# Optimization experiments

Measured on AMD Instinct MI355X. Metric: run time of the kernel, lower is better.

## Reference

```python
import jax, jax.numpy as jnp
import numpy as np
import math

S, B, H, NH, I, L, V, BK, MP = 512, 8, 768, 12, 2304, 4, 16384, 32, 512
DH = H // NH   # 64
DV = I // NH   # 192
EPS = 1e-7
SCALE = 1.0 / math.sqrt(3 * DH)


def make_log_bucket_position(relative_pos, bucket_size, max_position):
    sign = np.sign(relative_pos)
    mid = bucket_size // 2
    abs_pos = np.where((relative_pos < mid) & (relative_pos > -mid),
                       mid - 1,
                       np.clip(np.abs(relative_pos), None, max_position - 1))
    log_pos = np.ceil(np.log(abs_pos / mid) / math.log((max_position - 1) / mid) * (mid - 1)).astype(np.int64) + mid
    bucket_pos = np.where(abs_pos <= mid, relative_pos, log_pos * sign).astype(np.int64)
    return bucket_pos


def layer_norm(x, eps=EPS):
    m = jnp.mean(x, axis=-1, keepdims=True)
    v = jnp.var(x, axis=-1, keepdims=True)
    return (x - m) / jnp.sqrt(v + eps)


def setup_inputs() -> dict:
    key = jax.random.key(0)
    ks = jax.random.split(key, 10)
    std = math.sqrt(2.0 / (5.0 * H))
    inp = {}
    inp['input_ids'] = jax.random.randint(ks[0], (S, B), 0, V, dtype=jnp.int32)
    inp['attention_mask'] = jnp.zeros((B, 1, 1, S), dtype=bool)
    rel = np.arange(S)[:, None] - np.arange(S)[None, :]
    rel = make_log_bucket_position(rel, BK, MP)
    inp['position_indices'] = jnp.asarray(BK - 1 + rel, dtype=jnp.int32)  # [S,S] in [0, 2*BK-2]
    inp['word_emb'] = jax.random.normal(ks[1], (V, H), jnp.float32) * std
    inp['rel_emb'] = jax.random.normal(ks[2], (2 * BK - 1, H), jnp.float32) * std
    inp['rel_ln_w'] = jnp.ones((H,), jnp.float32)
    inp['rel_ln_b'] = jnp.zeros((H,), jnp.float32)
    inp['Wv'] = jax.random.normal(ks[3], (L, 2 * I, H), jnp.float32) * std
    inp['Wqk'] = jax.random.normal(ks[4], (L, 2 * H, H), jnp.float32) * std
    inp['bqk'] = jnp.zeros((L, 2 * H), jnp.float32)
    inp['Wo'] = jax.random.normal(ks[5], (L, H, I), jnp.float32) * std
    inp['l_skip'] = jnp.zeros((L, I), jnp.float32)
    return inp


def attention_glu_layer(x, mask, rel, pos_idx, Wv, Wqk, bqk, Wo, l_skip):
    # x: [S,B,H]; rel: [2*BK-1, H]; mask: [B,1,1,S] bool (True = masked)
    h = layer_norm(x)
    vg = jnp.einsum('sbh,ih->sbi', h, Wv)                  # [S,B,2I]
    value, gate = jnp.split(vg, 2, axis=-1)
    gate = jax.nn.gelu(gate, approximate=False)
    value_skip = jax.nn.gelu(value, approximate=False)
    qk = jnp.einsum('sbh,ih->sbi', h, Wqk) + bqk            # [S,B,2H]
    q, k = jnp.split(qk, 2, axis=-1)
    # relative position projections
    pos = rel @ Wqk.T + bqk                                 # [2*BK-1, 2H]
    pos = pos[pos_idx]                                      # [S,S,2H]
    q_pos, k_pos = jnp.split(pos, 2, axis=-1)
    q_pos = q_pos.reshape(S, S, NH, DH)
    k_pos = k_pos.reshape(S, S, NH, DH)
    q4 = q.reshape(S, B, NH, DH)
    k4 = k.reshape(S, B, NH, DH)
    v4 = value.reshape(S, B, NH, DV)
    scores = jnp.einsum('qbhd,kbhd->bhqk', q4, k4) * SCALE
    scores = scores + jnp.einsum('qbhd,qkhd->bhqk', q4, k_pos) * SCALE
    scores = scores + jnp.einsum('kbhd,qkhd->bhqk', k4, q_pos) * SCALE
    scores = jnp.where(mask, -jnp.inf, scores)
    probs = jax.nn.softmax(scores, axis=-1)
    probs = jnp.where(mask, 0.0, probs)
    ctx = jnp.einsum('bhqk,kbhv->qbhv', probs, v4).reshape(S, B, I)
    ctx = ctx + jax.nn.sigmoid(l_skip) * value_skip
    ctx = ctx * gate
    ctx = layer_norm(ctx)
    out = jnp.einsum('sbi,hi->sbh', ctx, Wo)
    return x + out


def reference(input_ids, attention_mask, position_indices, word_emb, rel_emb,
              rel_ln_w, rel_ln_b, Wv, Wqk, bqk, Wo, l_skip):
    x = layer_norm(word_emb[input_ids])                      # [S,B,H]
    rel = layer_norm(rel_emb) * rel_ln_w + rel_ln_b          # [2*BK-1, H]
    for l in range(L):
        x = attention_glu_layer(x, attention_mask, rel, position_indices,
                                Wv[l], Wqk[l], bqk[l], Wo[l], l_skip[l])
    return x
```

## Files before the change

### kernel.cpp

```cpp
#include <hip/hip_runtime.h>
#include <hip/hip_bf16.h>
#include <math.h>

#define S 512
#define B 8
#define H 768
#define NH 12
#define DH 64
#define DV 192
#define II 2304
#define NL 4
#define SCALE 0.07216878364870322f
#define EPS 1e-7f

#define NW0 (2*II*H)
#define NW1 (2*H*H)
#define NW2 (H*II)

typedef __attribute__((ext_vector_type(8))) short short8;
typedef __attribute__((ext_vector_type(4))) float f32x4;

__device__ __forceinline__ float b2f(ushort u){
  union { float f; unsigned int u; } v; v.u = ((unsigned int)u) << 16; return v.f;
}
__device__ __forceinline__ ushort f2b(float f){
  union { float f; unsigned int u; } v; v.f = f;
  unsigned int u = v.u;
  return (ushort)((u + 0x7fffu + ((u >> 16) & 1u)) >> 16);
}
__device__ __forceinline__ float gelu_f(float x){
  return 0.5f * x * (1.0f + erff(x * 0.70710678118654752f));
}
__device__ __forceinline__ void async_copy16(const ushort* g, ushort* l){
  __builtin_amdgcn_global_load_lds(
      (const __attribute__((address_space(1))) void*)g,
      (__attribute__((address_space(3))) void*)l, 16, 0, 0);
}

__device__ __forceinline__ void block_sum2(float& s, float& s2, float* red, int t){
  #pragma unroll
  for(int off=32; off>=1; off>>=1){ s += __shfl_xor(s, off); s2 += __shfl_xor(s2, off); }
  int w = t >> 6;
  if((t & 63) == 0){ red[w] = s; red[4 + w] = s2; }
  __syncthreads();
  s  = red[0] + red[1] + red[2] + red[3];
  s2 = red[4] + red[5] + red[6] + red[7];
}

__global__ __launch_bounds__(256)
void f2b3_kernel(const float* __restrict__ in0, const float* __restrict__ in1,
                 const float* __restrict__ in2, ushort* __restrict__ out){
  int i = (blockIdx.x * 256 + threadIdx.x) * 4;
  const float* src; int off;
  if(i < NW0){ src = in0; off = i; }
  else if(i < NW0+NW1){ src = in1; off = i - NW0; }
  else { src = in2; off = i - NW0 - NW1; }
  float4 v = *(const float4*)(src + off);
  __attribute__((aligned(8))) ushort tmp[4] = { f2b(v.x), f2b(v.y), f2b(v.z), f2b(v.w) };
  *(uint2*)(out + i) = *(const uint2*)tmp;
}

__global__ __launch_bounds__(256)
void embed_ln_kernel(const int* __restrict__ ids, const float* __restrict__ wemb,
                     float* __restrict__ x)
{
  __shared__ float red[8];
  const int sb = blockIdx.x, t = threadIdx.x;
  const float* row = wemb + (size_t)ids[sb] * H;
  float v0 = row[t], v1 = row[t+256], v2 = row[t+512];
  float s = v0+v1+v2, s2 = v0*v0+v1*v1+v2*v2;
  block_sum2(s, s2, red, t);
  float mean = s * (1.0f/H);
  float rstd = rsqrtf(s2*(1.0f/H) - mean*mean + EPS);
  float* xo = x + (size_t)sb * H;
  xo[t]     = (v0-mean)*rstd;
  xo[t+256] = (v1-mean)*rstd;
  xo[t+512] = (v2-mean)*rstd;
}

__global__ __launch_bounds__(256)
void rel_ln_kernel(const float* __restrict__ rel_emb, const float* __restrict__ w,
                   const float* __restrict__ bia, ushort* __restrict__ outb)
{
  __shared__ float red[8];
  const int j = blockIdx.x, t = threadIdx.x;
  const float* row = rel_emb + (size_t)j * H;
  float v0=row[t], v1=row[t+256], v2=row[t+512];
  float s=v0+v1+v2, s2=v0*v0+v1*v1+v2*v2;
  block_sum2(s,s2,red,t);
  float mean = s*(1.0f/H);
  float rstd = rsqrtf(s2*(1.0f/H)-mean*mean+EPS);
  ushort* o = outb + (size_t)j*H;
  o[t]     = f2b((v0-mean)*rstd * w[t]     + bia[t]);
  o[t+256] = f2b((v1-mean)*rstd * w[t+256] + bia[t+256]);
  o[t+512] = f2b((v2-mean)*rstd * w[t+512] + bia[t+512]);
}

__global__ __launch_bounds__(256)
void ln_x_kernel(const float* __restrict__ x, ushort* __restrict__ h)
{
  __shared__ float red[8];
  const int sb = blockIdx.x, t = threadIdx.x;
  const float* row = x + (size_t)sb * H;
  float v0 = row[t], v1 = row[t+256], v2 = row[t+512];
  float s = v0+v1+v2, s2 = v0*v0+v1*v1+v2*v2;
  block_sum2(s, s2, red, t);
  float mean = s * (1.0f/H);
  float rstd = rsqrtf(s2*(1.0f/H) - mean*mean + EPS);
  ushort* o = h + (size_t)sb * H;
  o[t]     = f2b((v0-mean)*rstd);
  o[t+256] = f2b((v1-mean)*rstd);
  o[t+512] = f2b((v2-mean)*rstd);
}

__global__ __launch_bounds__(256)
void gemm_nt64(const ushort* __restrict__ A, const ushort* __restrict__ Bw,
               const float* __restrict__ bias, ushort* __restrict__ Cout,
               int M, int N, int K)
{
  __shared__ ushort As[64][40];
  __shared__ ushort Bs[64][40];
  const int n0 = blockIdx.x * 64, m0 = blockIdx.y * 64;
  const int t = threadIdx.x;
  const int lrow = t >> 2, lk = (t & 3) * 8;
  const int lane = t & 63, w = t >> 6, lr = lane & 15, lq = lane >> 4;
  const int wr = (w >> 1) * 32, wc = (w & 1) * 32;
  f32x4 z = {0.f,0.f,0.f,0.f};
  f32x4 acc[2][2] = {{z,z},{z,z}};
  const int arow = m0 + lrow;
  const ushort* aptr = A  + (size_t)arow * K + lk;
  const ushort* bptr = Bw + (size_t)(n0 + lrow) * K + lk;
  for(int k0 = 0; k0 < K; k0 += 32){
    short8 av = {0,0,0,0,0,0,0,0};
    if(arow < M) av = *(const short8*)(aptr + k0);
    short8 bv = *(const short8*)(bptr + k0);
    __syncthreads();
    *(short8*)&As[lrow][lk] = av;
    *(short8*)&Bs[lrow][lk] = bv;
    __syncthreads();
    short8 a0 = *(const short8*)&As[wr + lr][lq * 8];
    short8 a1 = *(const short8*)&As[wr + 16 + lr][lq * 8];
    short8 b0 = *(const short8*)&Bs[wc + lr][lq * 8];
    short8 b1 = *(const short8*)&Bs[wc + 16 + lr][lq * 8];
    acc[0][0] = __builtin_amdgcn_mfma_f32_16x16x32_bf16(a0, b0, acc[0][0], 0,0,0);
    acc[0][1] = __builtin_amdgcn_mfma_f32_16x16x32_bf16(a0, b1, acc[0][1], 0,0,0);
    acc[1][0] = __builtin_amdgcn_mfma_f32_16x16x32_bf16(a1, b0, acc[1][0], 0,0,0);
    acc[1][1] = __builtin_amdgcn_mfma_f32_16x16x32_bf16(a1, b1, acc[1][1], 0,0,0);
  }
  #pragma unroll
  for(int i=0;i<2;i++){
    #pragma unroll
    for(int j=0;j<2;j++){
      #pragma unroll
      for(int r=0;r<4;r++){
        int m = m0 + wr + i*16 + lq*4 + r;
        int n = n0 + wc + j*16 + lr;
        if(m >= M) continue;
        float v = acc[i][j][r];
        if(bias) v += bias[n];
        Cout[(size_t)m*N + n] = f2b(v);
      }
    }
  }
}

template<int OUT_MODE>
__global__ __launch_bounds__(256)
void gemm128(const ushort* __restrict__ A, const ushort* __restrict__ Bw,
             const float* __restrict__ bias, void* __restrict__ Cout,
             int M, int N, int K)
{
  __shared__ ushort As[128*32];
  __shared__ ushort Bs[128*32];
  const int t = threadIdx.x, w = t>>6, lane = t&63, lr = lane&15, lq = lane>>4;
  const int m0 = blockIdx.y*128, n0 = blockIdx.x*128;
  const int wr = (w>>1)*64, wc = (w&1)*64;
  const int srow = (w*2)*16 + (lane>>2);
  const int sk = (lane&3)*8;
  const ushort* aG = A  + (size_t)(m0+srow)*K + sk;
  const ushort* bG = Bw + (size_t)(n0+srow)*K + sk;
  ushort* aL0 = As + (w*2)*512;
  ushort* aL1 = As + (w*2+1)*512;
  ushort* bL0 = Bs + (w*2)*512;
  ushort* bL1 = Bs + (w*2+1)*512;
  f32x4 z = {0.f,0.f,0.f,0.f};
  f32x4 acc[4][4] = {{z,z,z,z},{z,z,z,z},{z,z,z,z},{z,z,z,z}};
  for(int k0 = 0; k0 < K; k0 += 32){
    __syncthreads();
    async_copy16(aG + k0,                 aL0);
    async_copy16(aG + k0 + (size_t)16*K,  aL1);
    async_copy16(bG + k0,                 bL0);
    async_copy16(bG + k0 + (size_t)16*K,  bL1);
    __syncthreads();
    short8 af[4], bf[4];
    #pragma unroll
    for(int i=0;i<4;i++) af[i] = *(const short8*)&As[(wr + i*16 + lr)*32 + lq*8];
    #pragma unroll
    for(int j=0;j<4;j++) bf[j] = *(const short8*)&Bs[(wc + j*16 + lr)*32 + lq*8];
    #pragma unroll
    for(int i=0;i<4;i++)
      #pragma unroll
      for(int j=0;j<4;j++)
        acc[i][j] = __builtin_amdgcn_mfma_f32_16x16x32_bf16(af[i], bf[j], acc[i][j], 0,0,0);
  }
  #pragma unroll
  for(int i=0;i<4;i++){
    #pragma unroll
    for(int j=0;j<4;j++){
      #pragma unroll
      for(int r=0;r<4;r++){
        int m = m0 + wr + i*16 + lq*4 + r;
        int n = n0 + wc + j*16 + lr;
        float v = acc[i][j][r];
        if(bias) v += bias[n];
        if(OUT_MODE == 0)      ((float*) Cout)[(size_t)m*N + n] = v;
        else if(OUT_MODE == 1) ((ushort*)Cout)[(size_t)m*N + n] = f2b(v);
        else                   ((float*) Cout)[(size_t)m*N + n] += v;
      }
    }
  }
}

__global__ __launch_bounds__(256)
void gemm_vgqk(const ushort* __restrict__ A, const ushort* __restrict__ Ww,
               const float* __restrict__ bqk, ushort* __restrict__ vg,
               ushort* __restrict__ qk)
{
  const int K = H;
  __shared__ ushort As[128*32];
  __shared__ ushort Bs[128*32];
  const int t = threadIdx.x, w = t>>6, lane = t&63, lr = lane&15, lq = lane>>4;
  const int m0 = blockIdx.y*128, n0 = blockIdx.x*128;
  const int wr = (w>>1)*64, wc = (w&1)*64;
  const int srow = (w*2)*16 + (lane>>2);
  const int sk = (lane&3)*8;
  const ushort* aG = A  + (size_t)(m0+srow)*K + sk;
  const ushort* bG = Ww + (size_t)(n0+srow)*K + sk;
  ushort* aL0 = As + (w*2)*512;
  ushort* aL1 = As + (w*2+1)*512;
  ushort* bL0 = Bs + (w*2)*512;
  ushort* bL1 = Bs + (w*2+1)*512;
  f32x4 z = {0.f,0.f,0.f,0.f};
  f32x4 acc[4][4] = {{z,z,z,z},{z,z,z,z},{z,z,z,z},{z,z,z,z}};
  for(int k0 = 0; k0 < K; k0 += 32){
    __syncthreads();
    async_copy16(aG + k0,                 aL0);
    async_copy16(aG + k0 + (size_t)16*K,  aL1);
    async_copy16(bG + k0,                 bL0);
    async_copy16(bG + k0 + (size_t)16*K,  bL1);
    __syncthreads();
    short8 af[4], bf[4];
    #pragma unroll
    for(int i=0;i<4;i++) af[i] = *(const short8*)&As[(wr + i*16 + lr)*32 + lq*8];
    #pragma unroll
    for(int j=0;j<4;j++) bf[j] = *(const short8*)&Bs[(wc + j*16 + lr)*32 + lq*8];
    #pragma unroll
    for(int i=0;i<4;i++)
      #pragma unroll
      for(int j=0;j<4;j++)
        acc[i][j] = __builtin_amdgcn_mfma_f32_16x16x32_bf16(af[i], bf[j], acc[i][j], 0,0,0);
  }
  const bool is_qk = (n0 >= 2*II);
  #pragma unroll
  for(int i=0;i<4;i++){
    #pragma unroll
    for(int j=0;j<4;j++){
      #pragma unroll
      for(int r=0;r<4;r++){
        int m = m0 + wr + i*16 + lq*4 + r;
        int n = n0 + wc + j*16 + lr;
        float v = acc[i][j][r];
        if(is_qk){
          int nq = n - 2*II;
          qk[(size_t)m*(2*H) + nq] = f2b(v + bqk[nq]);
        } else {
          vg[(size_t)m*(2*II) + n] = f2b(v);
        }
      }
    }
  }
}

__global__ __launch_bounds__(256)
void cpq_mfma2_kernel(const ushort* __restrict__ qk, const ushort* __restrict__ posb,
                      ushort* __restrict__ cpT, ushort* __restrict__ cqT)
{
  const int kc = blockIdx.x;
  const int bh = blockIdx.y;
  const int bb = bh / NH, h = bh - bb*NH;
  const int which = blockIdx.z;
  const int t = threadIdx.x, w = t>>6, lane = t&63, lr = lane&15, lq = lane>>4;
  const ushort* ab = posb + (size_t)(w*16 + lr)*1536 + (which ? 0 : 768) + h*64;
  short8 a0 = *(const short8*)(ab + lq*8);
  short8 a1 = *(const short8*)(ab + 32 + lq*8);
  f32x4 z = {0.f,0.f,0.f,0.f};
  f32x4 acc[8] = {z,z,z,z,z,z,z,z};
  #pragma unroll
  for(int nt=0; nt<8; nt++){
    const int k = kc*128 + nt*16 + lr;
    const ushort* bp = qk + ((size_t)k*B + bb)*1536 + (which ? 768 : 0) + h*64;
    short8 b0 = *(const short8*)(bp + lq*8);
    short8 b1 = *(const short8*)(bp + 32 + lq*8);
    acc[nt] = __builtin_amdgcn_mfma_f32_16x16x32_bf16(a0, b0, acc[nt], 0,0,0);
    acc[nt] = __builtin_amdgcn_mfma_f32_16x16x32_bf16(a1, b1, acc[nt], 0,0,0);
  }
  ushort* outp = which ? cqT : cpT;
  #pragma unroll
  for(int nt=0; nt<8; nt++){
    #pragma unroll
    for(int r=0;r<4;r++){
      int j = w*16 + lq*4 + r;
      int k = kc*128 + nt*16 + lr;
      outp[((size_t)bh*64 + j)*512 + k] = f2b(acc[nt][r]);
    }
  }
}

__global__ __launch_bounds__(256)
void vt_kernel(const ushort* __restrict__ vg, ushort* __restrict__ vt)
{
  const int st = blockIdx.x, hh = blockIdx.y, b = blockIdx.z;
  __shared__ ushort tile[32][200];
  const int t = threadIdx.x;
  {
    int sl = t >> 3, v0 = (t & 7) * 24;
    const ushort* src = vg + ((size_t)((st*32 + sl)*B + b))*(2*II) + hh*DV + v0;
    *(short8*)&tile[sl][v0]      = *(const short8*)(src);
    *(short8*)&tile[sl][v0 + 8]  = *(const short8*)(src + 8);
    *(short8*)&tile[sl][v0 + 16] = *(const short8*)(src + 16);
  }
  __syncthreads();
  if(t < DV){
    __attribute__((aligned(16))) ushort tmp[32];
    #pragma unroll
    for(int s2=0;s2<32;s2++) tmp[s2] = tile[s2][t];
    ushort* dst = vt + (((size_t)(b*NH + hh))*DV + t)*S + st*32;
    #pragma unroll
    for(int c=0;c<32;c+=8) *(short8*)(dst + c) = *(const short8*)&tmp[c];
  }
}

__global__ __launch_bounds__(256)
void attn_kernel(const ushort* __restrict__ qk, const ushort* __restrict__ vt,
                 const ushort* __restrict__ cpT, const ushort* __restrict__ cqT,
                 const int* __restrict__ pidx, ushort* __restrict__ ctx)
{
  const int bh = blockIdx.x, qt = blockIdx.y;
  const int b = bh / NH, hh = bh - b*NH;
  __shared__ ushort Qs[32][72];
  __shared__ ushort Ps[32][520];
  __shared__ float cps[32][65];
  __shared__ float redm[4][32];
  __shared__ float reds[4][32];
  __shared__ float rowinv[32];
  const int t = threadIdx.x, w = t>>6, lane = t&63, lr = lane&15, lq = lane>>4;

  for(int i=t; i<512; i+=256){
    int r = i >> 4, d0 = (i & 15) * 4;
    const ushort* src = qk + ((size_t)((qt*32 + r)*B + b))*1536 + hh*DH + d0;
    *(uint2*)&Qs[r][d0] = *(const uint2*)src;
  }
  for(int i=t; i<32*64; i+=256){
    int j = i >> 5, r = i & 31;
    cps[r][j] = b2f(cpT[((size_t)bh*64 + j)*512 + qt*32 + r]);
  }
  __syncthreads();

  short8 a00 = *(const short8*)&Qs[lr][lq*8];
  short8 a01 = *(const short8*)&Qs[lr][32 + lq*8];
  short8 a10 = *(const short8*)&Qs[16 + lr][lq*8];
  short8 a11 = *(const short8*)&Qs[16 + lr][32 + lq*8];

  float sc[8][8];
  const int kbase = w * 128;
  const ushort* cqbase = cqT + (size_t)bh*64*512;
  f32x4 z4 = {0.f,0.f,0.f,0.f};
  #pragma unroll
  for(int tile=0; tile<8; tile++){
    const int k0 = kbase + tile*16;
    const ushort* kp = qk + ((size_t)((k0 + lr)*B + b))*1536 + H + hh*DH + lq*8;
    short8 b0 = *(const short8*)kp;
    short8 b1 = *(const short8*)(kp + 32);
    f32x4 acc[2] = {z4, z4};
    acc[0] = __builtin_amdgcn_mfma_f32_16x16x32_bf16(a00, b0, acc[0], 0,0,0);
    acc[0] = __builtin_amdgcn_mfma_f32_16x16x32_bf16(a01, b1, acc[0], 0,0,0);
    acc[1] = __builtin_amdgcn_mfma_f32_16x16x32_bf16(a10, b0, acc[1], 0,0,0);
    acc[1] = __builtin_amdgcn_mfma_f32_16x16x32_bf16(a11, b1, acc[1], 0,0,0);
    const int kcol = k0 + lr;
    #pragma unroll
    for(int qs=0;qs<2;qs++){
      #pragma unroll
      for(int r=0;r<4;r++){
        int ql = qs*16 + lq*4 + r;
        int pi = pidx[(qt*32+ql)*S + kcol];
        sc[tile][qs*4+r] = (acc[qs][r] + cps[ql][pi]
                       + b2f(cqbase[(size_t)pi*512 + kcol])) * SCALE;
      }
    }
  }

  float gm[8];
  #pragma unroll
  for(int j=0;j<8;j++){
    float m = sc[0][j];
    #pragma unroll
    for(int tile=1;tile<8;tile++) m = fmaxf(m, sc[tile][j]);
    #pragma unroll
    for(int off=1; off<16; off<<=1) m = fmaxf(m, __shfl_xor(m, off));
    if(lr==0) redm[w][(j>>2)*16 + lq*4 + (j&3)] = m;
  }
  __syncthreads();
  #pragma unroll
  for(int j=0;j<8;j++){
    int ql = (j>>2)*16 + lq*4 + (j&3);
    gm[j] = fmaxf(fmaxf(redm[0][ql],redm[1][ql]),fmaxf(redm[2][ql],redm[3][ql]));
  }
  #pragma unroll
  for(int j=0;j<8;j++){
    float s = 0.f;
    #pragma unroll
    for(int tile=0;tile<8;tile++){ float e = __expf(sc[tile][j]-gm[j]); sc[tile][j]=e; s+=e; }
    #pragma unroll
    for(int off=1; off<16; off<<=1) s += __shfl_xor(s, off);
    if(lr==0) reds[w][(j>>2)*16 + lq*4 + (j&3)] = s;
  }
  __syncthreads();
  #pragma unroll
  for(int j=0;j<8;j++){
    int ql = (j>>2)*16 + lq*4 + (j&3);
    float g = reds[0][ql]+reds[1][ql]+reds[2][ql]+reds[3][ql];
    if(w==0 && lr==0) rowinv[ql] = 1.0f/g;
  }
  #pragma unroll
  for(int tile=0;tile<8;tile++){
    #pragma unroll
    for(int j=0;j<8;j++){
      int ql = (j>>2)*16 + lq*4 + (j&3);
      Ps[ql][kbase + tile*16 + lr] = f2b(sc[tile][j]);
    }
  }
  __syncthreads();

  f32x4 acc2[2][3] = {{z4,z4,z4},{z4,z4,z4}};
  const ushort* vbase = vt + ((size_t)bh)*DV*S;
  #pragma unroll 4
  for(int kk=0; kk<S; kk+=32){
    short8 p0 = *(const short8*)&Ps[lr][kk + lq*8];
    short8 p1 = *(const short8*)&Ps[16 + lr][kk + lq*8];
    #pragma unroll
    for(int ti=0; ti<3; ti++){
      const int v0 = (w*3 + ti)*16;
      short8 bv = *(const short8*)(vbase + (size_t)(v0 + lr)*S + kk + lq*8);
      acc2[0][ti] = __builtin_amdgcn_mfma_f32_16x16x32_bf16(p0, bv, acc2[0][ti], 0,0,0);
      acc2[1][ti] = __builtin_amdgcn_mfma_f32_16x16x32_bf16(p1, bv, acc2[1][ti], 0,0,0);
    }
  }
  #pragma unroll
  for(int qs=0;qs<2;qs++){
    #pragma unroll
    for(int ti=0; ti<3; ti++){
      const int v0 = (w*3 + ti)*16;
      #pragma unroll
      for(int r=0;r<4;r++){
        int ql = qs*16 + lq*4 + r;
        float val = acc2[qs][ti][r] * rowinv[ql];
        ctx[((size_t)((qt*32+ql)*B + b))*II + hh*DV + v0 + lr] = f2b(val);
      }
    }
  }
}

__global__ __launch_bounds__(256)
void glu_ln_kernel(const ushort* __restrict__ ctx, const ushort* __restrict__ vg,
                   const float* __restrict__ ls, ushort* __restrict__ outb)
{
  __shared__ float red[8];
  const int sb = blockIdx.x, t = threadIdx.x;
  const ushort* crow = ctx + (size_t)sb*II;
  const ushort* vrow = vg + (size_t)sb*2*II;
  float c[9]; float s=0.f, s2=0.f;
  #pragma unroll
  for(int i=0;i<9;i++){
    int idx = t + i*256;
    float cv  = b2f(crow[idx]);
    float val = b2f(vrow[idx]);
    float gt  = b2f(vrow[II + idx]);
    float sk  = 1.0f/(1.0f + __expf(-ls[idx]));
    cv = (cv + sk*gelu_f(val)) * gelu_f(gt);
    c[i]=cv; s+=cv; s2+=cv*cv;
  }
  block_sum2(s,s2,red,t);
  float mean = s*(1.0f/II);
  float rstd = rsqrtf(s2*(1.0f/II)-mean*mean+EPS);
  ushort* o = outb + (size_t)sb*II;
  #pragma unroll
  for(int i=0;i<9;i++) o[t+i*256] = f2b((c[i]-mean)*rstd);
}

__global__ __launch_bounds__(256)
void copy_kernel(const float* __restrict__ x, float* __restrict__ out){
  int i = (blockIdx.x*256 + threadIdx.x)*4;
  *(float4*)(out + i) = *(const float4*)(x + i);
}

extern "C" void kernel_launch(void* const* d_in, const int* in_sizes, int n_in,
                              void* d_out, int out_size, void* d_ws, size_t ws_size,
                              hipStream_t stream)
{
  (void)in_sizes; (void)n_in; (void)out_size; (void)ws_size;
  const int* ids      = (const int*)d_in[0];
  const int* pidx     = (const int*)d_in[2];
  const float* wemb   = (const float*)d_in[3];
  const float* rele   = (const float*)d_in[4];
  const float* rlw    = (const float*)d_in[5];
  const float* rlb    = (const float*)d_in[6];
  const float* Wv     = (const float*)d_in[7];
  const float* Wqk    = (const float*)d_in[8];
  const float* bqk    = (const float*)d_in[9];
  const float* Wo     = (const float*)d_in[10];
  const float* lskip  = (const float*)d_in[11];

  char* wsb = (char*)d_ws;
  float*  x     = (float*) (wsb + 0);
  ushort* h     = (ushort*)(wsb + 12582912);
  ushort* relb  = (ushort*)(wsb + 18874368);
  ushort* posb  = (ushort*)(wsb + 18972672);
  ushort* vg    = (ushort*)(wsb + 19169280);
  ushort* qk    = (ushort*)(wsb + 56918016);
  ushort* cpT   = (ushort*)(wsb + 69500928);
  ushort* cqT   = (ushort*)(wsb + 75792384);
  ushort* ctx   = (ushort*)(wsb + 82083840);
  ushort* vt    = (ushort*)(wsb + 100958208);
  ushort* ctxln = vt;
  ushort* wvqk  = (ushort*)(wsb + 119832576);
  ushort* wqkb  = wvqk + (size_t)NW0;
  ushort* wob   = wvqk + (size_t)(NW0 + NW1);

  embed_ln_kernel<<<S*B, 256, 0, stream>>>(ids, wemb, x);
  rel_ln_kernel<<<63, 256, 0, stream>>>(rele, rlw, rlb, relb);

  for(int l=0; l<NL; l++){
    const float* Wv_l  = Wv  + (size_t)l * NW0;
    const float* Wqk_l = Wqk + (size_t)l * NW1;
    const float* bqk_l = bqk + (size_t)l * (2*H);
    const float* Wo_l  = Wo  + (size_t)l * NW2;
    const float* ls_l  = lskip + (size_t)l * II;

    f2b3_kernel<<<(NW0+NW1+NW2)/1024, 256, 0, stream>>>(Wv_l, Wqk_l, Wo_l, wvqk);

    ln_x_kernel<<<S*B, 256, 0, stream>>>(x, h);
    gemm_vgqk<<<dim3((2*II+2*H)/128, (S*B)/128), 256, 0, stream>>>(h, wvqk, bqk_l, vg, qk);
    gemm_nt64<<<dim3((2*H)/64, 1), 256, 0, stream>>>(relb, wqkb, bqk_l, posb, 63, 2*H, H);
    cpq_mfma2_kernel<<<dim3(S/128, B*NH, 2), 256, 0, stream>>>(qk, posb, cpT, cqT);
    vt_kernel<<<dim3(S/32, NH, B), 256, 0, stream>>>(vg, vt);
    attn_kernel<<<dim3(B*NH, S/32), 256, 0, stream>>>(qk, vt, cpT, cqT, pidx, ctx);
    glu_ln_kernel<<<S*B, 256, 0, stream>>>(ctx, vg, ls_l, ctxln);
    gemm128<2><<<dim3(H/128, (S*B)/128), 256, 0, stream>>>(ctxln, wob, nullptr, x, S*B, H, II);
  }
  copy_kernel<<<(S*B*H)/1024, 256, 0, stream>>>(x, (float*)d_out);
}
```

Measured before the change: 1.339 ms.

## Double K-step per barrier in GEMMs and merge V-transpose with position-score kernel

Both 128x128 GEMM kernels now stage two 32-wide K slices into separate shared buffers per barrier pair, which halves the number of __syncthreads and gives each load phase more outstanding copies. The V-transpose and the content-to-position MFMA kernels are merged into one launch that branches on block index, saving a launch and letting the two kinds of work run in the same grid. The small position GEMM is also launched before the large vg/qk GEMM. The cost is doubled LDS per GEMM block, which may lower occupancy, and load and compute are still not overlapped within an iteration.

```diff
diff --git a/kernel.cpp b/kernel.cpp
--- a/kernel.cpp
+++ b/kernel.cpp
@@ -170,8 +170,8 @@
              const float* __restrict__ bias, void* __restrict__ Cout,
              int M, int N, int K)
 {
-  __shared__ ushort As[128*32];
-  __shared__ ushort Bs[128*32];
+  __shared__ ushort As[2][128*32];
+  __shared__ ushort Bs[2][128*32];
   const int t = threadIdx.x, w = t>>6, lane = t&63, lr = lane&15, lq = lane>>4;
   const int m0 = blockIdx.y*128, n0 = blockIdx.x*128;
   const int wr = (w>>1)*64, wc = (w&1)*64;
@@ -179,29 +179,31 @@
   const int sk = (lane&3)*8;
   const ushort* aG = A  + (size_t)(m0+srow)*K + sk;
   const ushort* bG = Bw + (size_t)(n0+srow)*K + sk;
-  ushort* aL0 = As + (w*2)*512;
-  ushort* aL1 = As + (w*2+1)*512;
-  ushort* bL0 = Bs + (w*2)*512;
-  ushort* bL1 = Bs + (w*2+1)*512;
   f32x4 z = {0.f,0.f,0.f,0.f};
   f32x4 acc[4][4] = {{z,z,z,z},{z,z,z,z},{z,z,z,z},{z,z,z,z}};
-  for(int k0 = 0; k0 < K; k0 += 32){
-    __syncthreads();
-    async_copy16(aG + k0,                 aL0);
-    async_copy16(aG + k0 + (size_t)16*K,  aL1);
-    async_copy16(bG + k0,                 bL0);
-    async_copy16(bG + k0 + (size_t)16*K,  bL1);
-    __syncthreads();
-    short8 af[4], bf[4];
-    #pragma unroll
-    for(int i=0;i<4;i++) af[i] = *(const short8*)&As[(wr + i*16 + lr)*32 + lq*8];
-    #pragma unroll
-    for(int j=0;j<4;j++) bf[j] = *(const short8*)&Bs[(wc + j*16 + lr)*32 + lq*8];
-    #pragma unroll
-    for(int i=0;i<4;i++)
-      #pragma unroll
-      for(int j=0;j<4;j++)
-        acc[i][j] = __builtin_amdgcn_mfma_f32_16x16x32_bf16(af[i], bf[j], acc[i][j], 0,0,0);
+  for(int k0 = 0; k0 < K; k0 += 64){
+    __syncthreads();
+    #pragma unroll
+    for(int s=0;s<2;s++){
+      async_copy16(aG + k0 + s*32,                 As[s] + (w*2)*512);
+      async_copy16(aG + k0 + s*32 + (size_t)16*K,  As[s] + (w*2+1)*512);
+      async_copy16(bG + k0 + s*32,                 Bs[s] + (w*2)*512);
+      async_copy16(bG + k0 + s*32 + (size_t)16*K,  Bs[s] + (w*2+1)*512);
+    }
+    __syncthreads();
+    #pragma unroll
+    for(int s=0;s<2;s++){
+      short8 af[4], bf[4];
+      #pragma unroll
+      for(int i=0;i<4;i++) af[i] = *(const short8*)&As[s][(wr + i*16 + lr)*32 + lq*8];
+      #pragma unroll
+      for(int j=0;j<4;j++) bf[j] = *(const short8*)&Bs[s][(wc + j*16 + lr)*32 + lq*8];
+      #pragma unroll
+      for(int i=0;i<4;i++)
+        #pragma unroll
+        for(int j=0;j<4;j++)
+          acc[i][j] = __builtin_amdgcn_mfma_f32_16x16x32_bf16(af[i], bf[j], acc[i][j], 0,0,0);
+    }
   }
   #pragma unroll
   for(int i=0;i<4;i++){
@@ -227,8 +229,8 @@
                ushort* __restrict__ qk)
 {
   const int K = H;
-  __shared__ ushort As[128*32];
-  __shared__ ushort Bs[128*32];
+  __shared__ ushort As[2][128*32];
+  __shared__ ushort Bs[2][128*32];
   const int t = threadIdx.x, w = t>>6, lane = t&63, lr = lane&15, lq = lane>>4;
   const int m0 = blockIdx.y*128, n0 = blockIdx.x*128;
   const int wr = (w>>1)*64, wc = (w&1)*64;
@@ -236,29 +238,31 @@
   const int sk = (lane&3)*8;
   const ushort* aG = A  + (size_t)(m0+srow)*K + sk;
   const ushort* bG = Ww + (size_t)(n0+srow)*K + sk;
-  ushort* aL0 = As + (w*2)*512;
-  ushort* aL1 = As + (w*2+1)*512;
-  ushort* bL0 = Bs + (w*2)*512;
-  ushort* bL1 = Bs + (w*2+1)*512;
   f32x4 z = {0.f,0.f,0.f,0.f};
   f32x4 acc[4][4] = {{z,z,z,z},{z,z,z,z},{z,z,z,z},{z,z,z,z}};
-  for(int k0 = 0; k0 < K; k0 += 32){
-    __syncthreads();
-    async_copy16(aG + k0,                 aL0);
-    async_copy16(aG + k0 + (size_t)16*K,  aL1);
-    async_copy16(bG + k0,                 bL0);
-    async_copy16(bG + k0 + (size_t)16*K,  bL1);
-    __syncthreads();
-    short8 af[4], bf[4];
-    #pragma unroll
-    for(int i=0;i<4;i++) af[i] = *(const short8*)&As[(wr + i*16 + lr)*32 + lq*8];
-    #pragma unroll
-    for(int j=0;j<4;j++) bf[j] = *(const short8*)&Bs[(wc + j*16 + lr)*32 + lq*8];
-    #pragma unroll
-    for(int i=0;i<4;i++)
-      #pragma unroll
-      for(int j=0;j<4;j++)
-        acc[i][j] = __builtin_amdgcn_mfma_f32_16x16x32_bf16(af[i], bf[j], acc[i][j], 0,0,0);
+  for(int k0 = 0; k0 < K; k0 += 64){
+    __syncthreads();
+    #pragma unroll
+    for(int s=0;s<2;s++){
+      async_copy16(aG + k0 + s*32,                 As[s] + (w*2)*512);
+      async_copy16(aG + k0 + s*32 + (size_t)16*K,  As[s] + (w*2+1)*512);
+      async_copy16(bG + k0 + s*32,                 Bs[s] + (w*2)*512);
+      async_copy16(bG + k0 + s*32 + (size_t)16*K,  Bs[s] + (w*2+1)*512);
+    }
+    __syncthreads();
+    #pragma unroll
+    for(int s=0;s<2;s++){
+      short8 af[4], bf[4];
+      #pragma unroll
+      for(int i=0;i<4;i++) af[i] = *(const short8*)&As[s][(wr + i*16 + lr)*32 + lq*8];
+      #pragma unroll
+      for(int j=0;j<4;j++) bf[j] = *(const short8*)&Bs[s][(wc + j*16 + lr)*32 + lq*8];
+      #pragma unroll
+      for(int i=0;i<4;i++)
+        #pragma unroll
+        for(int j=0;j<4;j++)
+          acc[i][j] = __builtin_amdgcn_mfma_f32_16x16x32_bf16(af[i], bf[j], acc[i][j], 0,0,0);
+    }
   }
   const bool is_qk = (n0 >= 2*II);
   #pragma unroll
@@ -282,61 +286,64 @@
 }
 
 __global__ __launch_bounds__(256)
-void cpq_mfma2_kernel(const ushort* __restrict__ qk, const ushort* __restrict__ posb,
-                      ushort* __restrict__ cpT, ushort* __restrict__ cqT)
-{
-  const int kc = blockIdx.x;
-  const int bh = blockIdx.y;
-  const int bb = bh / NH, h = bh - bb*NH;
-  const int which = blockIdx.z;
-  const int t = threadIdx.x, w = t>>6, lane = t&63, lr = lane&15, lq = lane>>4;
-  const ushort* ab = posb + (size_t)(w*16 + lr)*1536 + (which ? 0 : 768) + h*64;
-  short8 a0 = *(const short8*)(ab + lq*8);
-  short8 a1 = *(const short8*)(ab + 32 + lq*8);
-  f32x4 z = {0.f,0.f,0.f,0.f};
-  f32x4 acc[8] = {z,z,z,z,z,z,z,z};
-  #pragma unroll
-  for(int nt=0; nt<8; nt++){
-    const int k = kc*128 + nt*16 + lr;
-    const ushort* bp = qk + ((size_t)k*B + bb)*1536 + (which ? 768 : 0) + h*64;
-    short8 b0 = *(const short8*)(bp + lq*8);
-    short8 b1 = *(const short8*)(bp + 32 + lq*8);
-    acc[nt] = __builtin_amdgcn_mfma_f32_16x16x32_bf16(a0, b0, acc[nt], 0,0,0);
-    acc[nt] = __builtin_amdgcn_mfma_f32_16x16x32_bf16(a1, b1, acc[nt], 0,0,0);
-  }
-  ushort* outp = which ? cqT : cpT;
-  #pragma unroll
-  for(int nt=0; nt<8; nt++){
-    #pragma unroll
-    for(int r=0;r<4;r++){
-      int j = w*16 + lq*4 + r;
-      int k = kc*128 + nt*16 + lr;
-      outp[((size_t)bh*64 + j)*512 + k] = f2b(acc[nt][r]);
-    }
-  }
-}
-
-__global__ __launch_bounds__(256)
-void vt_kernel(const ushort* __restrict__ vg, ushort* __restrict__ vt)
-{
-  const int st = blockIdx.x, hh = blockIdx.y, b = blockIdx.z;
+void vtcpq_kernel(const ushort* __restrict__ vg, ushort* __restrict__ vt,
+                  const ushort* __restrict__ qk, const ushort* __restrict__ posb,
+                  ushort* __restrict__ cpT, ushort* __restrict__ cqT)
+{
+  const int id = blockIdx.x;
+  const int t = threadIdx.x;
   __shared__ ushort tile[32][200];
-  const int t = threadIdx.x;
-  {
-    int sl = t >> 3, v0 = (t & 7) * 24;
-    const ushort* src = vg + ((size_t)((st*32 + sl)*B + b))*(2*II) + hh*DV + v0;
-    *(short8*)&tile[sl][v0]      = *(const short8*)(src);
-    *(short8*)&tile[sl][v0 + 8]  = *(const short8*)(src + 8);
-    *(short8*)&tile[sl][v0 + 16] = *(const short8*)(src + 16);
-  }
-  __syncthreads();
-  if(t < DV){
-    __attribute__((aligned(16))) ushort tmp[32];
-    #pragma unroll
-    for(int s2=0;s2<32;s2++) tmp[s2] = tile[s2][t];
-    ushort* dst = vt + (((size_t)(b*NH + hh))*DV + t)*S + st*32;
-    #pragma unroll
-    for(int c=0;c<32;c+=8) *(short8*)(dst + c) = *(const short8*)&tmp[c];
+  if(id < 1536){
+    const int st = id & 15;
+    const int hh = (id >> 4) % 12;
+    const int b  = id / 192;
+    {
+      int sl = t >> 3, v0 = (t & 7) * 24;
+      const ushort* src = vg + ((size_t)((st*32 + sl)*B + b))*(2*II) + hh*DV + v0;
+      *(short8*)&tile[sl][v0]      = *(const short8*)(src);
+      *(short8*)&tile[sl][v0 + 8]  = *(const short8*)(src + 8);
+      *(short8*)&tile[sl][v0 + 16] = *(const short8*)(src + 16);
+    }
+    __syncthreads();
+    if(t < DV){
+      __attribute__((aligned(16))) ushort tmp[32];
+      #pragma unroll
+      for(int s2=0;s2<32;s2++) tmp[s2] = tile[s2][t];
+      ushort* dst = vt + (((size_t)(b*NH + hh))*DV + t)*S + st*32;
+      #pragma unroll
+      for(int c=0;c<32;c+=8) *(short8*)(dst + c) = *(const short8*)&tmp[c];
+    }
+  } else {
+    const int jid = id - 1536;
+    const int kc = jid & 3;
+    const int bh = (jid >> 2) % 96;
+    const int which = jid / 384;
+    const int bb = bh / NH, h = bh - bb*NH;
+    const int w = t>>6, lane = t&63, lr = lane&15, lq = lane>>4;
+    const ushort* ab = posb + (size_t)(w*16 + lr)*1536 + (which ? 0 : 768) + h*64;
+    short8 a0 = *(const short8*)(ab + lq*8);
+    short8 a1 = *(const short8*)(ab + 32 + lq*8);
+    f32x4 z = {0.f,0.f,0.f,0.f};
+    f32x4 acc[8] = {z,z,z,z,z,z,z,z};
+    #pragma unroll
+    for(int nt=0; nt<8; nt++){
+      const int k = kc*128 + nt*16 + lr;
+      const ushort* bp = qk + ((size_t)k*B + bb)*1536 + (which ? 768 : 0) + h*64;
+      short8 b0 = *(const short8*)(bp + lq*8);
+      short8 b1 = *(const short8*)(bp + 32 + lq*8);
+      acc[nt] = __builtin_amdgcn_mfma_f32_16x16x32_bf16(a0, b0, acc[nt], 0,0,0);
+      acc[nt] = __builtin_amdgcn_mfma_f32_16x16x32_bf16(a1, b1, acc[nt], 0,0,0);
+    }
+    ushort* outp = which ? cqT : cpT;
+    #pragma unroll
+    for(int nt=0; nt<8; nt++){
+      #pragma unroll
+      for(int r=0;r<4;r++){
+        int j = w*16 + lq*4 + r;
+        int k = kc*128 + nt*16 + lr;
+        outp[((size_t)bh*64 + j)*512 + k] = f2b(acc[nt][r]);
+      }
+    }
   }
 }
 
@@ -547,12 +554,10 @@
     const float* ls_l  = lskip + (size_t)l * II;
 
     f2b3_kernel<<<(NW0+NW1+NW2)/1024, 256, 0, stream>>>(Wv_l, Wqk_l, Wo_l, wvqk);
-
     ln_x_kernel<<<S*B, 256, 0, stream>>>(x, h);
+    gemm_nt64<<<dim3((2*H)/64, 1), 256, 0, stream>>>(relb, wqkb, bqk_l, posb, 63, 2*H, H);
     gemm_vgqk<<<dim3((2*II+2*H)/128, (S*B)/128), 256, 0, stream>>>(h, wvqk, bqk_l, vg, qk);
-    gemm_nt64<<<dim3((2*H)/64, 1), 256, 0, stream>>>(relb, wqkb, bqk_l, posb, 63, 2*H, H);
-    cpq_mfma2_kernel<<<dim3(S/128, B*NH, 2), 256, 0, stream>>>(qk, posb, cpT, cqT);
-    vt_kernel<<<dim3(S/32, NH, B), 256, 0, stream>>>(vg, vt);
+    vtcpq_kernel<<<2304, 256, 0, stream>>>(vg, vt, qk, posb, cpT, cqT);
     attn_kernel<<<dim3(B*NH, S/32), 256, 0, stream>>>(qk, vt, cpT, cqT, pidx, ctx);
     glu_ln_kernel<<<S*B, 256, 0, stream>>>(ctx, vg, ls_l, ctxln);
     gemm128<2><<<dim3(H/128, (S*B)/128), 256, 0, stream>>>(ctxln, wob, nullptr, x, S*B, H, II);
```

Measured after the change: 1.258 ms. -6.0%, faster.
